# Kernel tuning notes

Hardware: AMD Instinct MI355X
Metric: run time of the kernel (lower is better)

The kernel has to match this reference:

```python
import jax, jax.numpy as jnp
import numpy as np

B, S, D, H = 4096, 200, 64, 36
BN_EPS = 1e-5
DICE_EPS = 1e-3


def setup_inputs() -> dict:
    key = jax.random.key(0)
    ks = jax.random.split(key, 6)
    return {
        "history": jax.random.normal(ks[0], (B, S, D), dtype=jnp.float32),
        "candidate": jax.random.normal(ks[1], (B, D), dtype=jnp.float32),
        "W1": jax.random.normal(ks[2], (4 * D, H), dtype=jnp.float32) * 0.05,
        "b1": jax.random.normal(ks[3], (H,), dtype=jnp.float32) * 0.05,
        "gamma": jnp.ones((H,), dtype=jnp.float32),
        "beta": jnp.zeros((H,), dtype=jnp.float32),
        "alpha": jax.random.normal(ks[4], (1,), dtype=jnp.float32),
        "W2": jax.random.normal(ks[5], (H, 1), dtype=jnp.float32) * 0.05,
        "b2": jnp.zeros((1,), dtype=jnp.float32),
    }


def reference(history, candidate, W1, b1, gamma, beta, alpha, W2, b2):
    b, s, d = history.shape
    cand = jnp.broadcast_to(candidate[:, None, :], (b, s, d))
    att_in = jnp.concatenate([cand, history, cand - history, cand * history], axis=-1)
    x = att_in.reshape(b * s, 4 * d)
    # Linear
    h = x @ W1 + b1
    # BatchNorm1d (training mode: batch statistics, biased variance)
    mu = h.mean(axis=0)
    var = h.var(axis=0)
    h = (h - mu) * jax.lax.rsqrt(var + BN_EPS) * gamma + beta
    # Dice: per-row normalization over features, eps=1e-3
    avg = h.mean(axis=1, keepdims=True)
    v = jnp.sum((h - avg) ** 2, axis=1, keepdims=True) / h.shape[1]
    ps = jax.nn.sigmoid((h - avg) / jnp.sqrt(v + DICE_EPS))
    h = ps * h + (1.0 - ps) * alpha * h
    # Output linear -> attention weight per (b, s)
    w = (h @ W2 + b2).reshape(b, s)
    # Weighted sum pooling over sequence
    return jnp.einsum("bs,bsd->bd", w, history)
```

## Files before the change

kernel.cpp:

```cpp
#include <hip/hip_runtime.h>
#include <hip/hip_bf16.h>
#include <math.h>

#define BB 4096
#define SS 200
#define DD 64
#define HH 36
#define NP 48
#define LDH 72
#define NROWSF (4096.0f * 200.0f)
#define NPB (2 * BB)
#define PSTRIDE 80
#define HSLOT 768

typedef short bf16x8 __attribute__((ext_vector_type(8)));
typedef float f32x4 __attribute__((ext_vector_type(4)));

__device__ __forceinline__ unsigned short f2bf(float f) {
    union { float f; unsigned u; } v; v.f = f;
    unsigned r = v.u + 0x7FFFu + ((v.u >> 16) & 1u);
    return (unsigned short)(r >> 16);
}
__device__ __forceinline__ unsigned f2bf2(float a, float b) {
    union { __hip_bfloat162 h; unsigned u; } v;
    v.h = __float22bfloat162_rn(float2{a, b});
    return v.u;
}
__device__ __forceinline__ float bf2f(unsigned short h) {
    union { unsigned u; float f; } v; v.u = (unsigned)h << 16;
    return v.f;
}
__device__ __forceinline__ float2 bf2x2(unsigned u) {
    union { unsigned q; float f; } a, b;
    a.q = u << 16; b.q = u & 0xFFFF0000u;
    return float2{a.f, b.f};
}

__global__ __launch_bounds__(256) void k_wb(const float* __restrict__ cand,
                                            const float* __restrict__ W1,
                                            const float* __restrict__ b1,
                                            unsigned short* __restrict__ WbG,
                                            float* __restrict__ baseG) {
    int b = blockIdx.x, t = threadIdx.x;
    __shared__ float shC[DD];
    if (t < DD) shC[t] = cand[b * DD + t];
    __syncthreads();
    unsigned short* wb = WbG + (size_t)b * (NP * DD);
#pragma unroll
    for (int u = 0; u < 12; ++u) {
        int e = t + u * 256;
        int n = e >> 6, k = e & 63;
        float val = 0.f;
        if (n < HH)
            val = W1[(DD + k) * HH + n] - W1[(2 * DD + k) * HH + n] +
                  shC[k] * W1[(3 * DD + k) * HH + n];
        wb[e] = f2bf(val);
    }
    if (t < NP) {
        float v = 0.f;
        if (t < HH) {
            v = b1[t];
            for (int k = 0; k < DD; ++k)
                v += shC[k] * (W1[k * HH + t] + W1[(2 * DD + k) * HH + t]);
        }
        baseG[b * NP + t] = v;
    }
}

template <bool WB>
__device__ __forceinline__ void prologue(int b, int half, int t,
                                         const float* __restrict__ hist,
                                         const float* __restrict__ cand,
                                         const float* __restrict__ W1,
                                         const float* __restrict__ b1,
                                         const unsigned short* __restrict__ WbG,
                                         const float* __restrict__ baseG,
                                         unsigned short* shH, unsigned short* shWbT,
                                         float* shC, float* shBase,
                                         float (*shBaseP)[NP]) {
    const float4* src =
        (const float4*)(hist + ((size_t)b * SS + (half ? 112 : 0)) * DD);
    float4 v[7];
    uint4 w0 = {}, w1 = {};
    float bse = 0.f;
    if (WB) {
        const uint4* wsrc = (const uint4*)(WbG + (size_t)b * (NP * DD));
        w0 = wsrc[t];
        if (t < 128) w1 = wsrc[256 + t];
        if (t < NP) bse = baseG[b * NP + t];
    } else {
        if (t < DD) shC[t] = cand[b * DD + t];
    }
    if (!half) {
#pragma unroll
        for (int u = 0; u < 7; ++u) v[u] = src[t + u * 256];
    } else {
#pragma unroll
        for (int u = 0; u < 5; ++u) v[u] = src[t + u * 256];
        if (t < 128) v[5] = src[t + 1280];
        *(unsigned*)&shH[(88 + (t >> 5)) * LDH + (t & 31) * 2] = 0;
    }
    if (!WB) __syncthreads();
#pragma unroll
    for (int u = 0; u < 7; ++u) {
        int i = t + u * 256;
        bool act = half ? (u < 5 || (u == 5 && t < 128)) : true;
        if (u < 6 || !half) {
            if (act) {
                int s = i >> 4, c = i & 15;
                uint2 o = {f2bf2(v[u].x, v[u].y), f2bf2(v[u].z, v[u].w)};
                *(uint2*)&shH[s * LDH + c * 4] = o;
            }
        }
    }
    if (WB) {
        *(uint4*)&shWbT[(t >> 3) * LDH + (t & 7) * 8] = w0;
        if (t < 128) *(uint4*)&shWbT[(32 + (t >> 3)) * LDH + (t & 7) * 8] = w1;
        if (t < NP) shBase[t] = bse;
        __syncthreads();
    } else {
        for (int e = t; e < NP * DD; e += 256) {
            int n = e >> 6, k = e & 63;
            float val = 0.f;
            if (n < HH)
                val = W1[(DD + k) * HH + n] - W1[(2 * DD + k) * HH + n] +
                      shC[k] * W1[(3 * DD + k) * HH + n];
            shWbT[n * LDH + k] = f2bf(val);
        }
        if (t < 4 * NP) {
            int g = t / NP, j = t - g * NP;
            float p = 0.f;
            if (j < HH) {
#pragma unroll 4
                for (int k = 16 * g; k < 16 * g + 16; ++k)
                    p += shC[k] * (W1[k * HH + j] + W1[(2 * DD + k) * HH + j]);
            }
            shBaseP[g][j] = p;
        }
        __syncthreads();
        if (t < NP) {
            float val = (t < HH) ? b1[t] : 0.f;
            shBase[t] = val + shBaseP[0][t] + shBaseP[1][t] + shBaseP[2][t] +
                        shBaseP[3][t];
        }
        __syncthreads();
    }
}

__device__ __forceinline__ void load_bfrags(const unsigned short* shWbT, int lane,
                                            bf16x8 (&bfr)[3][2]) {
    int col = lane & 15, q = lane >> 4;
#pragma unroll
    for (int nt = 0; nt < 3; ++nt)
#pragma unroll
        for (int kt = 0; kt < 2; ++kt)
            bfr[nt][kt] = *(const bf16x8*)&shWbT[(nt * 16 + col) * LDH + kt * 32 + q * 8];
}

__device__ __forceinline__ void gemm_tile(const unsigned short* shH,
                                          const bf16x8 (&bfr)[3][2], int mt, int lane,
                                          f32x4 (&d)[3]) {
    int m = mt * 16 + (lane & 15), q = lane >> 4;
    d[0] = f32x4{0.f, 0.f, 0.f, 0.f};
    d[1] = f32x4{0.f, 0.f, 0.f, 0.f};
    d[2] = f32x4{0.f, 0.f, 0.f, 0.f};
#pragma unroll
    for (int kt = 0; kt < 2; ++kt) {
        bf16x8 a = *(const bf16x8*)&shH[m * LDH + kt * 32 + q * 8];
#pragma unroll
        for (int nt = 0; nt < 3; ++nt)
            d[nt] = __builtin_amdgcn_mfma_f32_16x16x32_bf16(a, bfr[nt][kt], d[nt], 0, 0, 0);
    }
}

template <bool WB, bool RED, bool HS>
__global__ __launch_bounds__(256, 6) void k_pass1(const float* __restrict__ hist,
                                                  const float* __restrict__ cand,
                                                  const float* __restrict__ W1,
                                                  const float* __restrict__ b1,
                                                  const unsigned short* __restrict__ WbG,
                                                  const float* __restrict__ baseG,
                                                  unsigned short* __restrict__ hG,
                                                  float* __restrict__ pstat,
                                                  float* __restrict__ gsum,
                                                  float* __restrict__ gsum2) {
    __shared__ unsigned short shH[112 * LDH];
    __shared__ unsigned short shWbT[NP * LDH];
    __shared__ float shC[WB ? 1 : DD], shBase[NP];
    __shared__ float shBaseP[WB ? 1 : 4][NP];
    __shared__ float shP1[4][NP], shP2[4][NP];
    int bx = blockIdx.x, b = bx >> 1, half = bx & 1;
    int t = threadIdx.x, wave = t >> 6, lane = t & 63;
    int col = lane & 15, q = lane >> 4;

    prologue<WB>(b, half, t, hist, cand, W1, b1, WbG, baseG, shH, shWbT, shC,
                 shBase, shBaseP);

    bf16x8 bfr[3][2];
    load_bfrags(shWbT, lane, bfr);
    float basev[3];
#pragma unroll
    for (int nt = 0; nt < 3; ++nt) basev[nt] = shBase[nt * 16 + col];

    const int NTl = half ? 6 : 7;
    float cs1[3] = {0.f, 0.f, 0.f}, cs2[3] = {0.f, 0.f, 0.f};
    for (int mt = wave; mt < NTl; mt += 4) {
        f32x4 d[3];
        gemm_tile(shH, bfr, mt, lane, d);
        float vv[3][4];
#pragma unroll
        for (int nt = 0; nt < 3; ++nt)
#pragma unroll
            for (int r = 0; r < 4; ++r) vv[nt][r] = d[nt][r] + basev[nt];
        if (HS) {
            unsigned* hp = (unsigned*)(hG + ((size_t)bx * 7 + mt) * HSLOT);
#pragma unroll
            for (int nt = 0; nt < 3; ++nt) {
                hp[(nt * 2 + 0) * 64 + lane] = f2bf2(vv[nt][0], vv[nt][1]);
                hp[(nt * 2 + 1) * 64 + lane] = f2bf2(vv[nt][2], vv[nt][3]);
            }
        }
        if (half && mt == 5) {
            int grow0 = 192 + q * 4;
#pragma unroll
            for (int nt = 0; nt < 3; ++nt)
#pragma unroll
                for (int r = 0; r < 4; ++r)
                    if (grow0 + r < SS) {
                        cs1[nt] += vv[nt][r];
                        cs2[nt] += vv[nt][r] * vv[nt][r];
                    }
        } else {
#pragma unroll
            for (int nt = 0; nt < 3; ++nt)
#pragma unroll
                for (int r = 0; r < 4; ++r) {
                    cs1[nt] += vv[nt][r];
                    cs2[nt] += vv[nt][r] * vv[nt][r];
                }
        }
    }
#pragma unroll
    for (int nt = 0; nt < 3; ++nt) {
        cs1[nt] += __shfl_xor(cs1[nt], 16);
        cs1[nt] += __shfl_xor(cs1[nt], 32);
        cs2[nt] += __shfl_xor(cs2[nt], 16);
        cs2[nt] += __shfl_xor(cs2[nt], 32);
    }
    if (lane < 16) {
#pragma unroll
        for (int nt = 0; nt < 3; ++nt) {
            shP1[wave][nt * 16 + lane] = cs1[nt];
            shP2[wave][nt * 16 + lane] = cs2[nt];
        }
    }
    __syncthreads();
    if (RED) {
        if (t < HH)
            pstat[(size_t)bx * PSTRIDE + t] =
                shP1[0][t] + shP1[1][t] + shP1[2][t] + shP1[3][t];
        else if (t < 2 * HH) {
            int f = t - HH;
            pstat[(size_t)bx * PSTRIDE + t] =
                shP2[0][f] + shP2[1][f] + shP2[2][f] + shP2[3][f];
        }
    } else {
        if (t < HH) {
            atomicAdd(gsum + t, shP1[0][t] + shP1[1][t] + shP1[2][t] + shP1[3][t]);
            atomicAdd(gsum2 + t, shP2[0][t] + shP2[1][t] + shP2[2][t] + shP2[3][t]);
        }
    }
}

__global__ __launch_bounds__(256) void k_stats_red(const float* __restrict__ pstat,
                                                   const float* __restrict__ gamma,
                                                   const float* __restrict__ beta,
                                                   float* __restrict__ A,
                                                   float* __restrict__ Bc) {
    int f = blockIdx.x, t = threadIdx.x;
    if (f >= HH) {
        if (t == 0) { A[f] = 0.f; Bc[f] = 0.f; }
        return;
    }
    float s1 = 0.f, s2 = 0.f;
    for (int r = t; r < NPB; r += 256) {
        s1 += pstat[(size_t)r * PSTRIDE + f];
        s2 += pstat[(size_t)r * PSTRIDE + HH + f];
    }
#pragma unroll
    for (int off = 1; off < 64; off <<= 1) {
        s1 += __shfl_xor(s1, off);
        s2 += __shfl_xor(s2, off);
    }
    __shared__ float a1[4], a2[4];
    if ((t & 63) == 0) { a1[t >> 6] = s1; a2[t >> 6] = s2; }
    __syncthreads();
    if (t == 0) {
        s1 = a1[0] + a1[1] + a1[2] + a1[3];
        s2 = a2[0] + a2[1] + a2[2] + a2[3];
        float mu = s1 * (1.0f / NROWSF);
        float var = s2 * (1.0f / NROWSF) - mu * mu;
        float a = rsqrtf(var + 1e-5f) * gamma[f];
        A[f] = a;
        Bc[f] = beta[f] - mu * a;
    }
}

__global__ void k_stats(const float* __restrict__ gsum, const float* __restrict__ gsum2,
                        const float* __restrict__ gamma, const float* __restrict__ beta,
                        float* __restrict__ A, float* __restrict__ Bc) {
    int t = threadIdx.x;
    if (t < NP) {
        if (t < HH) {
            float mu = gsum[t] * (1.0f / NROWSF);
            float var = gsum2[t] * (1.0f / NROWSF) - mu * mu;
            float a = rsqrtf(var + 1e-5f) * gamma[t];
            A[t] = a;
            Bc[t] = beta[t] - mu * a;
        } else {
            A[t] = 0.f;
            Bc[t] = 0.f;
        }
    }
}

__global__ __launch_bounds__(256, 8) void k_pass3(const unsigned short* __restrict__ hG,
                                                  const float* __restrict__ hist,
                                                  const float* __restrict__ Acoef,
                                                  const float* __restrict__ Bcoef,
                                                  const float* __restrict__ alpha,
                                                  const float* __restrict__ W2,
                                                  const float* __restrict__ b2,
                                                  float* __restrict__ out) {
    __shared__ float shW[112];
    __shared__ float shPool[4][DD];
    int bx = blockIdx.x, b = bx >> 1, half = bx & 1;
    int t = threadIdx.x, wave = t >> 6, lane = t & 63;
    int col = lane & 15, q = lane >> 4;

    float Ar[3], Br[3], W2r[3];
#pragma unroll
    for (int nt = 0; nt < 3; ++nt) {
        int c = nt * 16 + col;
        Ar[nt] = Acoef[c];
        Br[nt] = Bcoef[c];
        W2r[nt] = (c < HH) ? W2[c] : 0.f;
    }
    float alv = alpha[0], one_m_alv = 1.0f - alv, b2v = b2[0];

    const int NTl = half ? 6 : 7;
    for (int mt = wave; mt < NTl; mt += 4) {
        const unsigned* hp = (const unsigned*)(hG + ((size_t)bx * 7 + mt) * HSLOT);
        float h[3][4];
#pragma unroll
        for (int nt = 0; nt < 3; ++nt) {
            float2 lo = bf2x2(hp[(nt * 2 + 0) * 64 + lane]);
            float2 hi = bf2x2(hp[(nt * 2 + 1) * 64 + lane]);
            h[nt][0] = fmaf(lo.x, Ar[nt], Br[nt]);
            h[nt][1] = fmaf(lo.y, Ar[nt], Br[nt]);
            h[nt][2] = fmaf(hi.x, Ar[nt], Br[nt]);
            h[nt][3] = fmaf(hi.y, Ar[nt], Br[nt]);
        }
        float s1[4], s2[4], wsum[4];
#pragma unroll
        for (int r = 0; r < 4; ++r) {
            s1[r] = h[0][r] + h[1][r] + h[2][r];
            s2[r] = h[0][r] * h[0][r] + h[1][r] * h[1][r] + h[2][r] * h[2][r];
            s1[r] += __shfl_xor(s1[r], 1);
            s1[r] += __shfl_xor(s1[r], 2);
            s1[r] += __shfl_xor(s1[r], 4);
            s1[r] += __shfl_xor(s1[r], 8);
            s2[r] += __shfl_xor(s2[r], 1);
            s2[r] += __shfl_xor(s2[r], 2);
            s2[r] += __shfl_xor(s2[r], 4);
            s2[r] += __shfl_xor(s2[r], 8);
        }
#pragma unroll
        for (int r = 0; r < 4; ++r) {
            float avg = s1[r] * (1.0f / (float)HH);
            float var = s2[r] * (1.0f / (float)HH) - avg * avg;
            float inv = rsqrtf(var + 1e-3f);
            float wv = 0.f;
#pragma unroll
            for (int nt = 0; nt < 3; ++nt) {
                float z = (h[nt][r] - avg) * inv;
                float ps = 1.0f / (1.0f + __expf(-z));
                float f = fmaf(ps, one_m_alv, alv);
                wv = fmaf(h[nt][r] * f, W2r[nt], wv);
            }
            wsum[r] = wv;
            wsum[r] += __shfl_xor(wsum[r], 1);
            wsum[r] += __shfl_xor(wsum[r], 2);
            wsum[r] += __shfl_xor(wsum[r], 4);
            wsum[r] += __shfl_xor(wsum[r], 8);
        }
        if (col == 0) {
            float4 o = {wsum[0] + b2v, wsum[1] + b2v, wsum[2] + b2v, wsum[3] + b2v};
            *(float4*)&shW[mt * 16 + q * 4] = o;
        }
    }
    __syncthreads();
    {
        const int rowLo = half ? 112 : 0, nR = half ? 88 : 112;
        const float* hb = hist + ((size_t)b * SS + rowLo) * DD;
        float p = 0.f;
        for (int s = wave; s < nR; s += 4)
            p = fmaf(shW[s], hb[(size_t)s * DD + lane], p);
        shPool[wave][lane] = p;
    }
    __syncthreads();
    if (t < DD)
        atomicAdd(out + b * DD + t,
                  shPool[0][t] + shPool[1][t] + shPool[2][t] + shPool[3][t]);
}

template <bool WB>
__global__ __launch_bounds__(256, 6) void k_pass2(const float* __restrict__ hist,
                                                  const float* __restrict__ cand,
                                                  const float* __restrict__ W1,
                                                  const float* __restrict__ b1,
                                                  const unsigned short* __restrict__ WbG,
                                                  const float* __restrict__ baseG,
                                                  const float* __restrict__ Acoef,
                                                  const float* __restrict__ Bcoef,
                                                  const float* __restrict__ alpha,
                                                  const float* __restrict__ W2,
                                                  const float* __restrict__ b2,
                                                  float* __restrict__ out) {
    __shared__ unsigned short shH[112 * LDH];
    __shared__ unsigned short shWbT[NP * LDH];
    __shared__ float shC[WB ? 1 : DD], shBase[NP];
    __shared__ float shBaseP[WB ? 1 : 4][NP];
    __shared__ float shW[112];
    __shared__ float shPool[4][DD];
    int bx = blockIdx.x, b = bx >> 1, half = bx & 1;
    int t = threadIdx.x, wave = t >> 6, lane = t & 63;
    int col = lane & 15, q = lane >> 4;

    prologue<WB>(b, half, t, hist, cand, W1, b1, WbG, baseG, shH, shWbT, shC,
                 shBase, shBaseP);

    bf16x8 bfr[3][2];
    load_bfrags(shWbT, lane, bfr);
    float baseAB[3], Ar[3], W2r[3];
#pragma unroll
    for (int nt = 0; nt < 3; ++nt) {
        int c = nt * 16 + col;
        Ar[nt] = Acoef[c];
        baseAB[nt] = fmaf(shBase[c], Ar[nt], Bcoef[c]);
        W2r[nt] = (c < HH) ? W2[c] : 0.f;
    }
    float alv = alpha[0], one_m_alv = 1.0f - alv, b2v = b2[0];

    const int NTl = half ? 6 : 7;
    for (int mt = wave; mt < NTl; mt += 4) {
        f32x4 d[3];
        gemm_tile(shH, bfr, mt, lane, d);
        float hp[3][4];
#pragma unroll
        for (int nt = 0; nt < 3; ++nt)
#pragma unroll
            for (int r = 0; r < 4; ++r)
                hp[nt][r] = fmaf(d[nt][r], Ar[nt], baseAB[nt]);
        float s1[4], s2[4], wsum[4];
#pragma unroll
        for (int r = 0; r < 4; ++r) {
            s1[r] = hp[0][r] + hp[1][r] + hp[2][r];
            s2[r] = hp[0][r] * hp[0][r] + hp[1][r] * hp[1][r] + hp[2][r] * hp[2][r];
            s1[r] += __shfl_xor(s1[r], 1);
            s1[r] += __shfl_xor(s1[r], 2);
            s1[r] += __shfl_xor(s1[r], 4);
            s1[r] += __shfl_xor(s1[r], 8);
            s2[r] += __shfl_xor(s2[r], 1);
            s2[r] += __shfl_xor(s2[r], 2);
            s2[r] += __shfl_xor(s2[r], 4);
            s2[r] += __shfl_xor(s2[r], 8);
        }
#pragma unroll
        for (int r = 0; r < 4; ++r) {
            float avg = s1[r] * (1.0f / (float)HH);
            float var = s2[r] * (1.0f / (float)HH) - avg * avg;
            float inv = rsqrtf(var + 1e-3f);
            float wv = 0.f;
#pragma unroll
            for (int nt = 0; nt < 3; ++nt) {
                float z = (hp[nt][r] - avg) * inv;
                float ps = 1.0f / (1.0f + __expf(-z));
                float f = fmaf(ps, one_m_alv, alv);
                wv = fmaf(hp[nt][r] * f, W2r[nt], wv);
            }
            wsum[r] = wv;
            wsum[r] += __shfl_xor(wsum[r], 1);
            wsum[r] += __shfl_xor(wsum[r], 2);
            wsum[r] += __shfl_xor(wsum[r], 4);
            wsum[r] += __shfl_xor(wsum[r], 8);
        }
        if (col == 0) {
            float4 o = {wsum[0] + b2v, wsum[1] + b2v, wsum[2] + b2v, wsum[3] + b2v};
            *(float4*)&shW[mt * 16 + q * 4] = o;
        }
    }
    __syncthreads();
    {
        const int nR = half ? 88 : 112;
        float p = 0.f;
        for (int s = wave; s < nR; s += 4)
            p = fmaf(shW[s], bf2f(shH[s * LDH + lane]), p);
        shPool[wave][lane] = p;
    }
    __syncthreads();
    if (t < DD)
        atomicAdd(out + b * DD + t,
                  shPool[0][t] + shPool[1][t] + shPool[2][t] + shPool[3][t]);
}

extern "C" void kernel_launch(void* const* d_in, const int* in_sizes, int n_in,
                              void* d_out, int out_size, void* d_ws, size_t ws_size,
                              hipStream_t stream) {
    const float* hist = (const float*)d_in[0];
    const float* cand = (const float*)d_in[1];
    const float* W1 = (const float*)d_in[2];
    const float* b1 = (const float*)d_in[3];
    const float* gamma = (const float*)d_in[4];
    const float* beta = (const float*)d_in[5];
    const float* alpha = (const float*)d_in[6];
    const float* W2 = (const float*)d_in[7];
    const float* b2 = (const float*)d_in[8];
    float* out = (float*)d_out;
    float* ws = (float*)d_ws;

    const size_t pstatF = (size_t)NPB * PSTRIDE;
    const size_t baseF = (size_t)BB * NP;
    const size_t wbS = (size_t)BB * NP * DD;
    const size_t hS = (size_t)NPB * 7 * HSLOT;
    const size_t hdrF = pstatF + 2 * NP + baseF;
    const size_t hstoreNeed = hdrF * 4 + (wbS + hS) * 2;
    const size_t fullNeed = hdrF * 4 + wbS * 2;
    const size_t midNeed = (pstatF + 2 * NP) * 4;

    hipMemsetAsync(out, 0, (size_t)out_size * sizeof(float), stream);
    if (ws_size >= hstoreNeed) {
        float* pstat = ws;
        float* A = pstat + pstatF;
        float* Bc = A + NP;
        float* baseG = Bc + NP;
        unsigned short* WbG = (unsigned short*)(baseG + baseF);
        unsigned short* hG = WbG + wbS;
        k_wb<<<BB, 256, 0, stream>>>(cand, W1, b1, WbG, baseG);
        k_pass1<true, true, true><<<NPB, 256, 0, stream>>>(
            hist, cand, W1, b1, WbG, baseG, hG, pstat, nullptr, nullptr);
        k_stats_red<<<NP, 256, 0, stream>>>(pstat, gamma, beta, A, Bc);
        k_pass3<<<NPB, 256, 0, stream>>>(hG, hist, A, Bc, alpha, W2, b2, out);
    } else if (ws_size >= fullNeed) {
        float* pstat = ws;
        float* A = pstat + pstatF;
        float* Bc = A + NP;
        float* baseG = Bc + NP;
        unsigned short* WbG = (unsigned short*)(baseG + baseF);
        k_wb<<<BB, 256, 0, stream>>>(cand, W1, b1, WbG, baseG);
        k_pass1<true, true, false><<<NPB, 256, 0, stream>>>(
            hist, cand, W1, b1, WbG, baseG, nullptr, pstat, nullptr, nullptr);
        k_stats_red<<<NP, 256, 0, stream>>>(pstat, gamma, beta, A, Bc);
        k_pass2<true><<<NPB, 256, 0, stream>>>(hist, cand, W1, b1, WbG, baseG, A, Bc,
                                               alpha, W2, b2, out);
    } else if (ws_size >= midNeed) {
        float* pstat = ws;
        float* A = pstat + pstatF;
        float* Bc = A + NP;
        k_pass1<false, true, false><<<NPB, 256, 0, stream>>>(
            hist, cand, W1, b1, nullptr, nullptr, nullptr, pstat, nullptr, nullptr);
        k_stats_red<<<NP, 256, 0, stream>>>(pstat, gamma, beta, A, Bc);
        k_pass2<false><<<NPB, 256, 0, stream>>>(hist, cand, W1, b1, nullptr, nullptr,
                                                A, Bc, alpha, W2, b2, out);
    } else {
        float* gsum = ws;
        float* gsum2 = ws + NP;
        float* A = ws + 2 * NP;
        float* Bc = ws + 3 * NP;
        hipMemsetAsync(gsum, 0, 2 * NP * sizeof(float), stream);
        k_pass1<false, false, false><<<NPB, 256, 0, stream>>>(
            hist, cand, W1, b1, nullptr, nullptr, nullptr, nullptr, gsum, gsum2);
        k_stats<<<1, 64, 0, stream>>>(gsum, gsum2, gamma, beta, A, Bc);
        k_pass2<false><<<NPB, 256, 0, stream>>>(hist, cand, W1, b1, nullptr, nullptr,
                                                A, Bc, alpha, W2, b2, out);
    }
}
```

Baseline: 467.0 us.

## Fuse pipeline into one persistent kernel with grid barriers for BatchNorm stats

Replaces the separate weight-prep, pass1, stats-reduce and pass3 launches with one persistent kernel of 1024 blocks, each handling four batch rows. Two software grid barriers built on atomics separate the statistics phase, the BN coefficient reduction and the Dice/pooling phase. Per-block output is written directly, which removes the output memset and the atomicAdd. This avoids launch overhead and the global Wb/base buffers, but relies on all 1024 blocks being co-resident, and it recomputes Wb per batch inside the kernel.

```diff
diff --git a/kernel.cpp b/kernel.cpp
--- a/kernel.cpp
+++ b/kernel.cpp
@@ -12,6 +12,8 @@
 #define NPB (2 * BB)
 #define PSTRIDE 80
 #define HSLOT 768
+#define GRID 1024
+#define BPB 4
 
 typedef short bf16x8 __attribute__((ext_vector_type(8)));
 typedef float f32x4 __attribute__((ext_vector_type(4)));
@@ -34,6 +36,331 @@
     union { unsigned q; float f; } a, b;
     a.q = u << 16; b.q = u & 0xFFFF0000u;
     return float2{a.f, b.f};
+}
+
+__device__ __forceinline__ void load_bfrags(const unsigned short* shWbT, int lane,
+                                            bf16x8 (&bfr)[3][2]) {
+    int col = lane & 15, q = lane >> 4;
+#pragma unroll
+    for (int nt = 0; nt < 3; ++nt)
+#pragma unroll
+        for (int kt = 0; kt < 2; ++kt)
+            bfr[nt][kt] = *(const bf16x8*)&shWbT[(nt * 16 + col) * LDH + kt * 32 + q * 8];
+}
+
+__device__ __forceinline__ void gemm_tile(const unsigned short* shH,
+                                          const bf16x8 (&bfr)[3][2], int mt, int lane,
+                                          f32x4 (&d)[3]) {
+    int m = mt * 16 + (lane & 15), q = lane >> 4;
+    d[0] = f32x4{0.f, 0.f, 0.f, 0.f};
+    d[1] = f32x4{0.f, 0.f, 0.f, 0.f};
+    d[2] = f32x4{0.f, 0.f, 0.f, 0.f};
+#pragma unroll
+    for (int kt = 0; kt < 2; ++kt) {
+        bf16x8 a = *(const bf16x8*)&shH[m * LDH + kt * 32 + q * 8];
+#pragma unroll
+        for (int nt = 0; nt < 3; ++nt)
+            d[nt] = __builtin_amdgcn_mfma_f32_16x16x32_bf16(a, bfr[nt][kt], d[nt], 0, 0, 0);
+    }
+}
+
+__device__ __forceinline__ void gridbar(unsigned* ctr, unsigned goal) {
+    __syncthreads();
+    if (threadIdx.x == 0) {
+        __hip_atomic_fetch_add(ctr, 1u, __ATOMIC_RELEASE, __HIP_MEMORY_SCOPE_AGENT);
+        while (__hip_atomic_load(ctr, __ATOMIC_ACQUIRE, __HIP_MEMORY_SCOPE_AGENT) < goal)
+            __builtin_amdgcn_s_sleep(8);
+    }
+    __syncthreads();
+}
+
+__global__ __launch_bounds__(256, 5) void k_fused(
+    const float* __restrict__ hist, const float* __restrict__ cand,
+    const float* __restrict__ W1, const float* __restrict__ b1,
+    const float* __restrict__ gamma, const float* __restrict__ beta,
+    const float* __restrict__ alpha, const float* __restrict__ W2,
+    const float* __restrict__ b2, float* __restrict__ out,
+    unsigned short* __restrict__ hG, float* __restrict__ pstat,
+    float* __restrict__ Af, float* __restrict__ Bcf, unsigned* __restrict__ ctr) {
+    __shared__ __align__(16) char shBuf[112 * 64 * 4];
+    __shared__ __align__(16) char shMisc[2752];
+    unsigned short* shH = (unsigned short*)shBuf;
+    unsigned short* shWbT = (unsigned short*)(shBuf + 16128);
+    float* shF = (float*)shBuf;
+    float* shC = (float*)shMisc;
+    float* shBase = (float*)(shMisc + 256);
+    float(*shBaseP)[NP] = (float(*)[NP])(shMisc + 448);
+    float(*shP1)[NP] = (float(*)[NP])(shMisc + 1216);
+    float(*shP2)[NP] = (float(*)[NP])(shMisc + 1984);
+    float* shW = (float*)shMisc;
+    float(*shPool)[DD] = (float(*)[DD])(shMisc + 448);
+
+    const int blk = blockIdx.x, t = threadIdx.x, wave = t >> 6, lane = t & 63;
+    const int col = lane & 15, q = lane >> 4;
+
+    float cs1[3] = {0.f, 0.f, 0.f}, cs2[3] = {0.f, 0.f, 0.f};
+    for (int bi = 0; bi < BPB; ++bi) {
+        const int b = blk + bi * GRID;
+        __syncthreads();
+        if (t < DD) shC[t] = cand[b * DD + t];
+        __syncthreads();
+        for (int e = t; e < NP * DD; e += 256) {
+            int n = e >> 6, k = e & 63;
+            float val = 0.f;
+            if (n < HH)
+                val = W1[(DD + k) * HH + n] - W1[(2 * DD + k) * HH + n] +
+                      shC[k] * W1[(3 * DD + k) * HH + n];
+            shWbT[n * LDH + k] = f2bf(val);
+        }
+        if (t < 4 * NP) {
+            int g = t / NP, j = t - g * NP;
+            float p = 0.f;
+            if (j < HH) {
+#pragma unroll 4
+                for (int k = 16 * g; k < 16 * g + 16; ++k)
+                    p += shC[k] * (W1[k * HH + j] + W1[(2 * DD + k) * HH + j]);
+            }
+            shBaseP[g][j] = p;
+        }
+        __syncthreads();
+        if (t < NP) {
+            float val = (t < HH) ? b1[t] : 0.f;
+            shBase[t] = val + shBaseP[0][t] + shBaseP[1][t] + shBaseP[2][t] +
+                        shBaseP[3][t];
+        }
+        __syncthreads();
+        bf16x8 bfr[3][2];
+        load_bfrags(shWbT, lane, bfr);
+        float basev[3];
+#pragma unroll
+        for (int nt = 0; nt < 3; ++nt) basev[nt] = shBase[nt * 16 + col];
+
+        for (int half = 0; half < 2; ++half) {
+            if (half) __syncthreads();
+            const float4* src =
+                (const float4*)(hist + ((size_t)b * SS + (half ? 112 : 0)) * DD);
+            float4 v[7];
+            if (!half) {
+#pragma unroll
+                for (int u = 0; u < 7; ++u) v[u] = src[t + u * 256];
+            } else {
+#pragma unroll
+                for (int u = 0; u < 5; ++u) v[u] = src[t + u * 256];
+                if (t < 128) v[5] = src[t + 1280];
+                *(unsigned*)&shH[(88 + (t >> 5)) * LDH + (t & 31) * 2] = 0;
+            }
+#pragma unroll
+            for (int u = 0; u < 7; ++u) {
+                int i = t + u * 256;
+                bool act = half ? (u < 5 || (u == 5 && t < 128)) : true;
+                if (u < 6 || !half) {
+                    if (act) {
+                        int s = i >> 4, c = i & 15;
+                        uint2 o = {f2bf2(v[u].x, v[u].y), f2bf2(v[u].z, v[u].w)};
+                        *(uint2*)&shH[s * LDH + c * 4] = o;
+                    }
+                }
+            }
+            __syncthreads();
+            const int seg = (b << 1) | half;
+            const int NTl = half ? 6 : 7;
+            for (int mt = wave; mt < NTl; mt += 4) {
+                f32x4 d[3];
+                gemm_tile(shH, bfr, mt, lane, d);
+                float vv[3][4];
+#pragma unroll
+                for (int nt = 0; nt < 3; ++nt)
+#pragma unroll
+                    for (int r = 0; r < 4; ++r) vv[nt][r] = d[nt][r] + basev[nt];
+                uint2* hp2 = (uint2*)(hG + ((size_t)seg * 7 + mt) * HSLOT);
+#pragma unroll
+                for (int nt = 0; nt < 3; ++nt) {
+                    uint2 o = {f2bf2(vv[nt][0], vv[nt][1]), f2bf2(vv[nt][2], vv[nt][3])};
+                    hp2[nt * 64 + lane] = o;
+                }
+                if (half && mt == 5) {
+                    int grow0 = 192 + q * 4;
+#pragma unroll
+                    for (int nt = 0; nt < 3; ++nt)
+#pragma unroll
+                        for (int r = 0; r < 4; ++r)
+                            if (grow0 + r < SS) {
+                                cs1[nt] += vv[nt][r];
+                                cs2[nt] += vv[nt][r] * vv[nt][r];
+                            }
+                } else {
+#pragma unroll
+                    for (int nt = 0; nt < 3; ++nt)
+#pragma unroll
+                        for (int r = 0; r < 4; ++r) {
+                            cs1[nt] += vv[nt][r];
+                            cs2[nt] += vv[nt][r] * vv[nt][r];
+                        }
+                }
+            }
+        }
+    }
+#pragma unroll
+    for (int nt = 0; nt < 3; ++nt) {
+        cs1[nt] += __shfl_xor(cs1[nt], 16);
+        cs1[nt] += __shfl_xor(cs1[nt], 32);
+        cs2[nt] += __shfl_xor(cs2[nt], 16);
+        cs2[nt] += __shfl_xor(cs2[nt], 32);
+    }
+    __syncthreads();
+    if (lane < 16) {
+#pragma unroll
+        for (int nt = 0; nt < 3; ++nt) {
+            shP1[wave][nt * 16 + lane] = cs1[nt];
+            shP2[wave][nt * 16 + lane] = cs2[nt];
+        }
+    }
+    __syncthreads();
+    if (t < HH)
+        pstat[(size_t)blk * PSTRIDE + t] =
+            shP1[0][t] + shP1[1][t] + shP1[2][t] + shP1[3][t];
+    else if (t < 2 * HH) {
+        int f = t - HH;
+        pstat[(size_t)blk * PSTRIDE + t] =
+            shP2[0][f] + shP2[1][f] + shP2[2][f] + shP2[3][f];
+    }
+
+    gridbar(ctr + 0, GRID);
+
+    if (blk < NP) {
+        if (blk < HH) {
+            float s1 = 0.f, s2 = 0.f;
+#pragma unroll
+            for (int rr = 0; rr < GRID / 256; ++rr) {
+                int r = t + rr * 256;
+                s1 += pstat[(size_t)r * PSTRIDE + blk];
+                s2 += pstat[(size_t)r * PSTRIDE + HH + blk];
+            }
+#pragma unroll
+            for (int off = 1; off < 64; off <<= 1) {
+                s1 += __shfl_xor(s1, off);
+                s2 += __shfl_xor(s2, off);
+            }
+            __syncthreads();
+            if (lane == 0) { shP1[0][wave] = s1; shP1[0][4 + wave] = s2; }
+            __syncthreads();
+            if (t == 0) {
+                s1 = shP1[0][0] + shP1[0][1] + shP1[0][2] + shP1[0][3];
+                s2 = shP1[0][4] + shP1[0][5] + shP1[0][6] + shP1[0][7];
+                float mu = s1 * (1.0f / NROWSF);
+                float var = s2 * (1.0f / NROWSF) - mu * mu;
+                float a = rsqrtf(var + 1e-5f) * gamma[blk];
+                Af[blk] = a;
+                Bcf[blk] = beta[blk] - mu * a;
+            }
+        } else if (t == 0) {
+            Af[blk] = 0.f;
+            Bcf[blk] = 0.f;
+        }
+    }
+
+    gridbar(ctr + 1, GRID);
+
+    float Ar[3], Br[3], W2r[3];
+#pragma unroll
+    for (int nt = 0; nt < 3; ++nt) {
+        int c = nt * 16 + col;
+        Ar[nt] = Af[c];
+        Br[nt] = Bcf[c];
+        W2r[nt] = (c < HH) ? W2[c] : 0.f;
+    }
+    const float alv = alpha[0], one_m_alv = 1.0f - alv, b2v = b2[0];
+
+    for (int bi = 0; bi < BPB; ++bi) {
+        const int b = blk + bi * GRID;
+        float pacc = 0.f;
+        for (int half = 0; half < 2; ++half) {
+            __syncthreads();
+            const float4* src =
+                (const float4*)(hist + ((size_t)b * SS + (half ? 112 : 0)) * DD);
+            float4* dstF = (float4*)shF;
+            float4 v[7];
+            if (!half) {
+#pragma unroll
+                for (int u = 0; u < 7; ++u) v[u] = src[t + u * 256];
+#pragma unroll
+                for (int u = 0; u < 7; ++u) dstF[t + u * 256] = v[u];
+            } else {
+#pragma unroll
+                for (int u = 0; u < 5; ++u) v[u] = src[t + u * 256];
+                if (t < 128) v[5] = src[t + 1280];
+#pragma unroll
+                for (int u = 0; u < 5; ++u) dstF[t + u * 256] = v[u];
+                if (t < 128) dstF[t + 1280] = v[5];
+            }
+            const int seg = (b << 1) | half;
+            const int NTl = half ? 6 : 7;
+            for (int mt = wave; mt < NTl; mt += 4) {
+                const uint2* hp2 =
+                    (const uint2*)(hG + ((size_t)seg * 7 + mt) * HSLOT);
+                uint2 hr[3];
+#pragma unroll
+                for (int nt = 0; nt < 3; ++nt) hr[nt] = hp2[nt * 64 + lane];
+                float h[3][4];
+#pragma unroll
+                for (int nt = 0; nt < 3; ++nt) {
+                    float2 lo = bf2x2(hr[nt].x), hi = bf2x2(hr[nt].y);
+                    h[nt][0] = fmaf(lo.x, Ar[nt], Br[nt]);
+                    h[nt][1] = fmaf(lo.y, Ar[nt], Br[nt]);
+                    h[nt][2] = fmaf(hi.x, Ar[nt], Br[nt]);
+                    h[nt][3] = fmaf(hi.y, Ar[nt], Br[nt]);
+                }
+                float s1[4], s2[4], wsum[4];
+#pragma unroll
+                for (int r = 0; r < 4; ++r) {
+                    s1[r] = h[0][r] + h[1][r] + h[2][r];
+                    s2[r] = h[0][r] * h[0][r] + h[1][r] * h[1][r] + h[2][r] * h[2][r];
+                    s1[r] += __shfl_xor(s1[r], 1);
+                    s1[r] += __shfl_xor(s1[r], 2);
+                    s1[r] += __shfl_xor(s1[r], 4);
+                    s1[r] += __shfl_xor(s1[r], 8);
+                    s2[r] += __shfl_xor(s2[r], 1);
+                    s2[r] += __shfl_xor(s2[r], 2);
+                    s2[r] += __shfl_xor(s2[r], 4);
+                    s2[r] += __shfl_xor(s2[r], 8);
+                }
+#pragma unroll
+                for (int r = 0; r < 4; ++r) {
+                    float avg = s1[r] * (1.0f / (float)HH);
+                    float var = s2[r] * (1.0f / (float)HH) - avg * avg;
+                    float inv = rsqrtf(var + 1e-3f);
+                    float wv = 0.f;
+#pragma unroll
+                    for (int nt = 0; nt < 3; ++nt) {
+                        float z = (h[nt][r] - avg) * inv;
+                        float ps = 1.0f / (1.0f + __expf(-z));
+                        float f = fmaf(ps, one_m_alv, alv);
+                        wv = fmaf(h[nt][r] * f, W2r[nt], wv);
+                    }
+                    wsum[r] = wv;
+                    wsum[r] += __shfl_xor(wsum[r], 1);
+                    wsum[r] += __shfl_xor(wsum[r], 2);
+                    wsum[r] += __shfl_xor(wsum[r], 4);
+                    wsum[r] += __shfl_xor(wsum[r], 8);
+                }
+                if (col == 0) {
+                    float4 o = {wsum[0] + b2v, wsum[1] + b2v, wsum[2] + b2v,
+                                wsum[3] + b2v};
+                    *(float4*)&shW[mt * 16 + q * 4] = o;
+                }
+            }
+            __syncthreads();
+            const int nR = half ? 88 : 112;
+            for (int s = wave; s < nR; s += 4)
+                pacc = fmaf(shW[s], shF[s * DD + lane], pacc);
+        }
+        __syncthreads();
+        shPool[wave][lane] = pacc;
+        __syncthreads();
+        if (t < DD)
+            out[b * DD + t] =
+                shPool[0][t] + shPool[1][t] + shPool[2][t] + shPool[3][t];
+    }
 }
 
 __global__ __launch_bounds__(256) void k_wb(const float* __restrict__ cand,
@@ -147,40 +474,13 @@
     }
 }
 
-__device__ __forceinline__ void load_bfrags(const unsigned short* shWbT, int lane,
-                                            bf16x8 (&bfr)[3][2]) {
-    int col = lane & 15, q = lane >> 4;
-#pragma unroll
-    for (int nt = 0; nt < 3; ++nt)
-#pragma unroll
-        for (int kt = 0; kt < 2; ++kt)
-            bfr[nt][kt] = *(const bf16x8*)&shWbT[(nt * 16 + col) * LDH + kt * 32 + q * 8];
-}
-
-__device__ __forceinline__ void gemm_tile(const unsigned short* shH,
-                                          const bf16x8 (&bfr)[3][2], int mt, int lane,
-                                          f32x4 (&d)[3]) {
-    int m = mt * 16 + (lane & 15), q = lane >> 4;
-    d[0] = f32x4{0.f, 0.f, 0.f, 0.f};
-    d[1] = f32x4{0.f, 0.f, 0.f, 0.f};
-    d[2] = f32x4{0.f, 0.f, 0.f, 0.f};
-#pragma unroll
-    for (int kt = 0; kt < 2; ++kt) {
-        bf16x8 a = *(const bf16x8*)&shH[m * LDH + kt * 32 + q * 8];
-#pragma unroll
-        for (int nt = 0; nt < 3; ++nt)
-            d[nt] = __builtin_amdgcn_mfma_f32_16x16x32_bf16(a, bfr[nt][kt], d[nt], 0, 0, 0);
-    }
-}
-
-template <bool WB, bool RED, bool HS>
+template <bool WB, bool RED>
 __global__ __launch_bounds__(256, 6) void k_pass1(const float* __restrict__ hist,
                                                   const float* __restrict__ cand,
                                                   const float* __restrict__ W1,
                                                   const float* __restrict__ b1,
                                                   const unsigned short* __restrict__ WbG,
                                                   const float* __restrict__ baseG,
-                                                  unsigned short* __restrict__ hG,
                                                   float* __restrict__ pstat,
                                                   float* __restrict__ gsum,
                                                   float* __restrict__ gsum2) {
@@ -195,7 +495,6 @@
 
     prologue<WB>(b, half, t, hist, cand, W1, b1, WbG, baseG, shH, shWbT, shC,
                  shBase, shBaseP);
-
     bf16x8 bfr[3][2];
     load_bfrags(shWbT, lane, bfr);
     float basev[3];
@@ -207,19 +506,6 @@
     for (int mt = wave; mt < NTl; mt += 4) {
         f32x4 d[3];
         gemm_tile(shH, bfr, mt, lane, d);
-        float vv[3][4];
-#pragma unroll
-        for (int nt = 0; nt < 3; ++nt)
-#pragma unroll
-            for (int r = 0; r < 4; ++r) vv[nt][r] = d[nt][r] + basev[nt];
-        if (HS) {
-            unsigned* hp = (unsigned*)(hG + ((size_t)bx * 7 + mt) * HSLOT);
-#pragma unroll
-            for (int nt = 0; nt < 3; ++nt) {
-                hp[(nt * 2 + 0) * 64 + lane] = f2bf2(vv[nt][0], vv[nt][1]);
-                hp[(nt * 2 + 1) * 64 + lane] = f2bf2(vv[nt][2], vv[nt][3]);
-            }
-        }
         if (half && mt == 5) {
             int grow0 = 192 + q * 4;
 #pragma unroll
@@ -227,16 +513,18 @@
 #pragma unroll
                 for (int r = 0; r < 4; ++r)
                     if (grow0 + r < SS) {
-                        cs1[nt] += vv[nt][r];
-                        cs2[nt] += vv[nt][r] * vv[nt][r];
+                        float vv = d[nt][r] + basev[nt];
+                        cs1[nt] += vv;
+                        cs2[nt] += vv * vv;
                     }
         } else {
 #pragma unroll
             for (int nt = 0; nt < 3; ++nt)
 #pragma unroll
                 for (int r = 0; r < 4; ++r) {
-                    cs1[nt] += vv[nt][r];
-                    cs2[nt] += vv[nt][r] * vv[nt][r];
+                    float vv = d[nt][r] + basev[nt];
+                    cs1[nt] += vv;
+                    cs2[nt] += vv * vv;
                 }
         }
     }
@@ -322,96 +610,6 @@
             Bc[t] = 0.f;
         }
     }
-}
-
-__global__ __launch_bounds__(256, 8) void k_pass3(const unsigned short* __restrict__ hG,
-                                                  const float* __restrict__ hist,
-                                                  const float* __restrict__ Acoef,
-                                                  const float* __restrict__ Bcoef,
-                                                  const float* __restrict__ alpha,
-                                                  const float* __restrict__ W2,
-                                                  const float* __restrict__ b2,
-                                                  float* __restrict__ out) {
-    __shared__ float shW[112];
-    __shared__ float shPool[4][DD];
-    int bx = blockIdx.x, b = bx >> 1, half = bx & 1;
-    int t = threadIdx.x, wave = t >> 6, lane = t & 63;
-    int col = lane & 15, q = lane >> 4;
-
-    float Ar[3], Br[3], W2r[3];
-#pragma unroll
-    for (int nt = 0; nt < 3; ++nt) {
-        int c = nt * 16 + col;
-        Ar[nt] = Acoef[c];
-        Br[nt] = Bcoef[c];
-        W2r[nt] = (c < HH) ? W2[c] : 0.f;
-    }
-    float alv = alpha[0], one_m_alv = 1.0f - alv, b2v = b2[0];
-
-    const int NTl = half ? 6 : 7;
-    for (int mt = wave; mt < NTl; mt += 4) {
-        const unsigned* hp = (const unsigned*)(hG + ((size_t)bx * 7 + mt) * HSLOT);
-        float h[3][4];
-#pragma unroll
-        for (int nt = 0; nt < 3; ++nt) {
-            float2 lo = bf2x2(hp[(nt * 2 + 0) * 64 + lane]);
-            float2 hi = bf2x2(hp[(nt * 2 + 1) * 64 + lane]);
-            h[nt][0] = fmaf(lo.x, Ar[nt], Br[nt]);
-            h[nt][1] = fmaf(lo.y, Ar[nt], Br[nt]);
-            h[nt][2] = fmaf(hi.x, Ar[nt], Br[nt]);
-            h[nt][3] = fmaf(hi.y, Ar[nt], Br[nt]);
-        }
-        float s1[4], s2[4], wsum[4];
-#pragma unroll
-        for (int r = 0; r < 4; ++r) {
-            s1[r] = h[0][r] + h[1][r] + h[2][r];
-            s2[r] = h[0][r] * h[0][r] + h[1][r] * h[1][r] + h[2][r] * h[2][r];
-            s1[r] += __shfl_xor(s1[r], 1);
-            s1[r] += __shfl_xor(s1[r], 2);
-            s1[r] += __shfl_xor(s1[r], 4);
-            s1[r] += __shfl_xor(s1[r], 8);
-            s2[r] += __shfl_xor(s2[r], 1);
-            s2[r] += __shfl_xor(s2[r], 2);
-            s2[r] += __shfl_xor(s2[r], 4);
-            s2[r] += __shfl_xor(s2[r], 8);
-        }
-#pragma unroll
-        for (int r = 0; r < 4; ++r) {
-            float avg = s1[r] * (1.0f / (float)HH);
-            float var = s2[r] * (1.0f / (float)HH) - avg * avg;
-            float inv = rsqrtf(var + 1e-3f);
-            float wv = 0.f;
-#pragma unroll
-            for (int nt = 0; nt < 3; ++nt) {
-                float z = (h[nt][r] - avg) * inv;
-                float ps = 1.0f / (1.0f + __expf(-z));
-                float f = fmaf(ps, one_m_alv, alv);
-                wv = fmaf(h[nt][r] * f, W2r[nt], wv);
-            }
-            wsum[r] = wv;
-            wsum[r] += __shfl_xor(wsum[r], 1);
-            wsum[r] += __shfl_xor(wsum[r], 2);
-            wsum[r] += __shfl_xor(wsum[r], 4);
-            wsum[r] += __shfl_xor(wsum[r], 8);
-        }
-        if (col == 0) {
-            float4 o = {wsum[0] + b2v, wsum[1] + b2v, wsum[2] + b2v, wsum[3] + b2v};
-            *(float4*)&shW[mt * 16 + q * 4] = o;
-        }
-    }
-    __syncthreads();
-    {
-        const int rowLo = half ? 112 : 0, nR = half ? 88 : 112;
-        const float* hb = hist + ((size_t)b * SS + rowLo) * DD;
-        float p = 0.f;
-        for (int s = wave; s < nR; s += 4)
-            p = fmaf(shW[s], hb[(size_t)s * DD + lane], p);
-        shPool[wave][lane] = p;
-    }
-    __syncthreads();
-    if (t < DD)
-        atomicAdd(out + b * DD + t,
-                  shPool[0][t] + shPool[1][t] + shPool[2][t] + shPool[3][t]);
 }
 
 template <bool WB>
@@ -439,7 +637,6 @@
 
     prologue<WB>(b, half, t, hist, cand, W1, b1, WbG, baseG, shH, shWbT, shC,
                  shBase, shBaseP);
-
     bf16x8 bfr[3][2];
     load_bfrags(shWbT, lane, bfr);
     float baseAB[3], Ar[3], W2r[3];
@@ -529,37 +726,36 @@
     float* out = (float*)d_out;
     float* ws = (float*)d_ws;
 
+    const size_t ctrF = 4;
+    const size_t pstatFsd = (size_t)GRID * PSTRIDE;
+    const size_t hShorts = (size_t)NPB * 7 * HSLOT;
+    const size_t fusedNeed = (ctrF + pstatFsd + 2 * NP) * 4 + hShorts * 2;
+
     const size_t pstatF = (size_t)NPB * PSTRIDE;
     const size_t baseF = (size_t)BB * NP;
     const size_t wbS = (size_t)BB * NP * DD;
-    const size_t hS = (size_t)NPB * 7 * HSLOT;
-    const size_t hdrF = pstatF + 2 * NP + baseF;
-    const size_t hstoreNeed = hdrF * 4 + (wbS + hS) * 2;
-    const size_t fullNeed = hdrF * 4 + wbS * 2;
+    const size_t fullNeed = (pstatF + 2 * NP + baseF) * 4 + wbS * 2;
     const size_t midNeed = (pstatF + 2 * NP) * 4;
 
-    hipMemsetAsync(out, 0, (size_t)out_size * sizeof(float), stream);
-    if (ws_size >= hstoreNeed) {
-        float* pstat = ws;
-        float* A = pstat + pstatF;
+    if (ws_size >= fusedNeed) {
+        unsigned* ctr = (unsigned*)ws;
+        float* pstat = ws + ctrF;
+        float* A = pstat + pstatFsd;
         float* Bc = A + NP;
-        float* baseG = Bc + NP;
-        unsigned short* WbG = (unsigned short*)(baseG + baseF);
-        unsigned short* hG = WbG + wbS;
-        k_wb<<<BB, 256, 0, stream>>>(cand, W1, b1, WbG, baseG);
-        k_pass1<true, true, true><<<NPB, 256, 0, stream>>>(
-            hist, cand, W1, b1, WbG, baseG, hG, pstat, nullptr, nullptr);
-        k_stats_red<<<NP, 256, 0, stream>>>(pstat, gamma, beta, A, Bc);
-        k_pass3<<<NPB, 256, 0, stream>>>(hG, hist, A, Bc, alpha, W2, b2, out);
+        unsigned short* hG = (unsigned short*)(Bc + NP);
+        hipMemsetAsync(ctr, 0, ctrF * sizeof(unsigned), stream);
+        k_fused<<<GRID, 256, 0, stream>>>(hist, cand, W1, b1, gamma, beta, alpha,
+                                          W2, b2, out, hG, pstat, A, Bc, ctr);
     } else if (ws_size >= fullNeed) {
         float* pstat = ws;
         float* A = pstat + pstatF;
         float* Bc = A + NP;
         float* baseG = Bc + NP;
         unsigned short* WbG = (unsigned short*)(baseG + baseF);
+        hipMemsetAsync(out, 0, (size_t)out_size * sizeof(float), stream);
         k_wb<<<BB, 256, 0, stream>>>(cand, W1, b1, WbG, baseG);
-        k_pass1<true, true, false><<<NPB, 256, 0, stream>>>(
-            hist, cand, W1, b1, WbG, baseG, nullptr, pstat, nullptr, nullptr);
+        k_pass1<true, true><<<NPB, 256, 0, stream>>>(hist, cand, W1, b1, WbG, baseG,
+                                                     pstat, nullptr, nullptr);
         k_stats_red<<<NP, 256, 0, stream>>>(pstat, gamma, beta, A, Bc);
         k_pass2<true><<<NPB, 256, 0, stream>>>(hist, cand, W1, b1, WbG, baseG, A, Bc,
                                                alpha, W2, b2, out);
@@ -567,8 +763,9 @@
         float* pstat = ws;
         float* A = pstat + pstatF;
         float* Bc = A + NP;
-        k_pass1<false, true, false><<<NPB, 256, 0, stream>>>(
-            hist, cand, W1, b1, nullptr, nullptr, nullptr, pstat, nullptr, nullptr);
+        hipMemsetAsync(out, 0, (size_t)out_size * sizeof(float), stream);
+        k_pass1<false, true><<<NPB, 256, 0, stream>>>(hist, cand, W1, b1, nullptr,
+                                                      nullptr, pstat, nullptr, nullptr);
         k_stats_red<<<NP, 256, 0, stream>>>(pstat, gamma, beta, A, Bc);
         k_pass2<false><<<NPB, 256, 0, stream>>>(hist, cand, W1, b1, nullptr, nullptr,
                                                 A, Bc, alpha, W2, b2, out);
@@ -577,9 +774,10 @@
         float* gsum2 = ws + NP;
         float* A = ws + 2 * NP;
         float* Bc = ws + 3 * NP;
-        hipMemsetAsync(gsum, 0, 2 * NP * sizeof(float), stream);
-        k_pass1<false, false, false><<<NPB, 256, 0, stream>>>(
-            hist, cand, W1, b1, nullptr, nullptr, nullptr, nullptr, gsum, gsum2);
+        hipMemsetAsync(ws, 0, 2 * NP * sizeof(float), stream);
+        hipMemsetAsync(out, 0, (size_t)out_size * sizeof(float), stream);
+        k_pass1<false, false><<<NPB, 256, 0, stream>>>(hist, cand, W1, b1, nullptr,
+                                                       nullptr, nullptr, gsum, gsum2);
         k_stats<<<1, 64, 0, stream>>>(gsum, gsum2, gamma, beta, A, Bc);
         k_pass2<false><<<NPB, 256, 0, stream>>>(hist, cand, W1, b1, nullptr, nullptr,
                                                 A, Bc, alpha, W2, b2, out);
```

Result: slower. 796.2 us (+70.5%).
